# Kernel optimization log

Measured on AMD Instinct MI355X. Metric: run time of the kernel, lower is better.

Reference implementation:

```python
import jax, jax.numpy as jnp
import numpy as np

D = 1024        # d_hidden
DE = 512        # d_expert (routed)
E = 8           # n_routed_experts
TOP_K = 2
DS = DE * 2     # shared expert width = d_expert * n_shared_experts


def setup_inputs() -> dict:
    key = jax.random.key(0)
    ks = jax.random.split(key, 8)
    s = 1.0 / np.sqrt(D)
    return {
        "x": jax.random.normal(ks[0], (2, 1024, D), dtype=jnp.float32),
        "W_g": jax.random.normal(ks[1], (D, E), dtype=jnp.float32) * s,
        "Wg_e": jax.random.normal(ks[2], (E, D, DE), dtype=jnp.float32) * s,
        "Wu_e": jax.random.normal(ks[3], (E, D, DE), dtype=jnp.float32) * s,
        "Wd_e": jax.random.normal(ks[4], (E, DE, D), dtype=jnp.float32) * (1.0 / np.sqrt(DE)),
        "Wg_s": jax.random.normal(ks[5], (D, DS), dtype=jnp.float32) * s,
        "Wu_s": jax.random.normal(ks[6], (D, DS), dtype=jnp.float32) * s,
        "Wd_s": jax.random.normal(ks[7], (DS, D), dtype=jnp.float32) * (1.0 / np.sqrt(DS)),
    }


def _moe(x, W_g, Wg_e, Wu_e, Wd_e, Wg_s, Wu_s, Wd_s):
    B, T, Dm = x.shape
    N = B * T
    xf = x.reshape(N, Dm)

    # shared expert (SwiGLU)
    shared = (jax.nn.silu(xf @ Wg_s) * (xf @ Wu_s)) @ Wd_s  # [N, D]

    # gating: softmax then top-k (set membership identical to torch sorted=False)
    probs = jax.nn.softmax(xf @ W_g, axis=-1)               # [N, E]
    topk_vals, topk_ids = jax.lax.top_k(probs, TOP_K)       # [N, K]

    # combine weights c[n, e] = sum of topk_vals where routed to expert e
    # (equivalent to the original gather -> weighted scatter_add combine)
    c = jnp.zeros((N, E), dtype=x.dtype)
    c = c.at[jnp.arange(N)[:, None], topk_ids].add(topk_vals)

    # dense per-expert SwiGLU, weighted-combined (same math as gather/scatter loop)
    gate = jax.nn.silu(jnp.einsum('nd,edh->neh', xf, Wg_e))
    up = jnp.einsum('nd,edh->neh', xf, Wu_e)
    routed = jnp.einsum('neh,ne,ehd->nd', gate * up, c, Wd_e)  # [N, D]

    return (shared + routed).reshape(B, T, Dm)


def reference(x, W_g, Wg_e, Wu_e, Wd_e, Wg_s, Wu_s, Wd_s):
    return _moe(x, W_g, Wg_e, Wu_e, Wd_e, Wg_s, Wu_s, Wd_s)
```

## Files before the change

### kernel.cpp

```cpp
#include <hip/hip_runtime.h>
#include <hip/hip_bf16.h>

#define NTOK 2048
#define DIM  1024
#define DEXP 512
#define NEXP 8
#define DSH  1024
#define KH   5120
#define MAXROWS 5120
#define PACKBLOCKS 2560

typedef __hip_bfloat16 bf16;
typedef __attribute__((ext_vector_type(8))) short bf16x8;
typedef __attribute__((ext_vector_type(4))) float floatx4;

__device__ __forceinline__ void gl_lds16(const bf16* g, bf16* l) {
    __builtin_amdgcn_global_load_lds(
        (const __attribute__((address_space(1))) void*)g,
        (__attribute__((address_space(3))) void*)l, 16, 0, 0);
}

__device__ __forceinline__ float b2f(short s) {
    union { float f; unsigned u; } v;
    v.u = ((unsigned)(unsigned short)s) << 16;
    return v.f;
}

struct B4 { bf16 a, b, c, d; };

__global__ __launch_bounds__(128) void pack_gate(
        const float* __restrict__ Wg_s, const float* __restrict__ Wu_s,
        const float* __restrict__ Wg_e, const float* __restrict__ Wu_e,
        const float* __restrict__ x, const float* __restrict__ Wg,
        bf16* __restrict__ Bg, bf16* __restrict__ Bu,
        bf16* __restrict__ Xb, int2* __restrict__ te, float2* __restrict__ tp) {
    int b = blockIdx.x;
    const int tid = threadIdx.x;
    if (b < PACKBLOCKS) {
        __shared__ unsigned lt[64][35];
        const float* src; bf16* dst; int C; long dstBase; int tilesX;
        if (b < 256)        { src = Wg_s; dst = Bg; C = 1024; dstBase = 0; tilesX = 16; }
        else if (b < 1280)  { int z = (b - 256) >> 7; b = (b - 256) & 127;
                              src = Wg_e + (long)z * DIM * DEXP; dst = Bg; C = 512;
                              dstBase = (long)(DSH + z * DEXP) * 1024; tilesX = 8; }
        else if (b < 1536)  { b -= 1280; src = Wu_s; dst = Bu; C = 1024; dstBase = 0; tilesX = 16; }
        else                { int z = (b - 1536) >> 7; b = (b - 1536) & 127;
                              src = Wu_e + (long)z * DIM * DEXP; dst = Bu; C = 512;
                              dstBase = (long)(DSH + z * DEXP) * 1024; tilesX = 8; }
        const int tileX = b & (tilesX - 1), tileY = b / tilesX;
        const int c0 = tileX * 64, r0 = tileY * 64;

        const int lrow = tid >> 4, lch = tid & 15;
#pragma unroll
        for (int i = 0; i < 8; i++) {
            int row = lrow + i * 8;
            float4 v = *(const float4*)(src + (long)(r0 + row) * C + c0 + lch * 4);
            union { bf16 h[2]; unsigned u; } p0, p1;
            p0.h[0] = __float2bfloat16(v.x); p0.h[1] = __float2bfloat16(v.y);
            p1.h[0] = __float2bfloat16(v.z); p1.h[1] = __float2bfloat16(v.w);
            lt[row][lch * 2]     = p0.u;
            lt[row][lch * 2 + 1] = p1.u;
        }
        __syncthreads();
        const int kc = tid & 7;
#pragma unroll
        for (int i = 0; i < 4; i++) {
            int h = (tid >> 3) + i * 16;
            union { unsigned short s[8]; bf16x8 v8; } o;
#pragma unroll
            for (int j = 0; j < 8; j++)
                o.s[j] = ((const unsigned short*)lt[kc * 8 + j])[h];
            *(bf16x8*)(dst + dstBase + (long)(c0 + h) * 1024 + r0 + kc * 8) = o.v8;
        }
    } else {
        int t = (b - PACKBLOCKS) * 2 + (tid >> 6);
        int lane = tid & 63;
        const float* xr = x + (long)t * DIM;
        bf16* xo = Xb + (long)t * DIM;
        float acc[NEXP] = {0.f, 0.f, 0.f, 0.f, 0.f, 0.f, 0.f, 0.f};
#pragma unroll
        for (int i = 0; i < 4; i++) {
            int d = lane * 4 + i * 256;
            float4 xv = *(const float4*)(xr + d);
            B4 o{__float2bfloat16(xv.x), __float2bfloat16(xv.y),
                 __float2bfloat16(xv.z), __float2bfloat16(xv.w)};
            *(B4*)(xo + d) = o;
#pragma unroll
            for (int j = 0; j < 4; j++) {
                float xs = (j == 0) ? xv.x : (j == 1) ? xv.y : (j == 2) ? xv.z : xv.w;
                float4 w0 = *(const float4*)(Wg + (d + j) * NEXP);
                float4 w1 = *(const float4*)(Wg + (d + j) * NEXP + 4);
                acc[0] += xs * w0.x; acc[1] += xs * w0.y; acc[2] += xs * w0.z; acc[3] += xs * w0.w;
                acc[4] += xs * w1.x; acc[5] += xs * w1.y; acc[6] += xs * w1.z; acc[7] += xs * w1.w;
            }
        }
#pragma unroll
        for (int e = 0; e < NEXP; e++)
#pragma unroll
            for (int off = 32; off; off >>= 1)
                acc[e] += __shfl_xor(acc[e], off);
        if (lane == 0) {
            float m = acc[0];
#pragma unroll
            for (int e = 1; e < NEXP; e++) m = fmaxf(m, acc[e]);
            float p[NEXP], s = 0.f;
#pragma unroll
            for (int e = 0; e < NEXP; e++) { p[e] = expf(acc[e] - m); s += p[e]; }
            float inv = 1.f / s;
#pragma unroll
            for (int e = 0; e < NEXP; e++) p[e] *= inv;
            int i1 = 0;
#pragma unroll
            for (int e = 1; e < NEXP; e++) if (p[e] > p[i1]) i1 = e;
            int i2 = (i1 == 0) ? 1 : 0;
#pragma unroll
            for (int e = 0; e < NEXP; e++) if (e != i1 && p[e] > p[i2]) i2 = e;
            te[t] = make_int2(i1, i2);
            tp[t] = make_float2(p[i1], p[i2]);
        }
    }
}

__global__ __launch_bounds__(512) void assign_kernel(const int2* __restrict__ te,
                                                     const float2* __restrict__ tp,
                                                     int* __restrict__ counts,
                                                     int* __restrict__ offs,
                                                     int* __restrict__ tok_list,
                                                     float* __restrict__ cw,
                                                     int* __restrict__ s1a,
                                                     int* __restrict__ s2a) {
    __shared__ int cnt[NEXP];
    const int e = threadIdx.x >> 6;
    const int lane = threadIdx.x & 63;
    int base = 0;
    for (int t0 = 0; t0 < NTOK; t0 += 64) {
        int t = t0 + lane;
        int2 ee = te[t];
        bool m1 = (ee.x == e), m2 = (ee.y == e);
        bool mt = m1 || m2;
        unsigned long long mask = __ballot(mt);
        int pre = __popcll(mask & ((1ull << lane) - 1ull));
        if (mt) {
            int slot = base + pre;
            tok_list[e * NTOK + slot] = t;
            float2 pp = tp[t];
            cw[e * NTOK + slot] = m1 ? pp.x : pp.y;
            if (m1) s1a[t] = slot; else s2a[t] = slot;
        }
        base += __popcll(mask);
    }
    int rounded = (base + 127) & ~127;
    for (int s = base + lane; s < rounded; s += 64) {
        tok_list[e * NTOK + s] = 0;
        cw[e * NTOK + s] = 0.f;
    }
    if (lane == 0) cnt[e] = base;
    __syncthreads();
    if (threadIdx.x == 0) {
        int o = 0;
#pragma unroll
        for (int i = 0; i < NEXP; i++) {
            counts[i] = cnt[i];
            offs[i] = o;
            o += (cnt[i] + 127) & ~127;
        }
    }
}

__global__ __launch_bounds__(256) void gu_all(const bf16* __restrict__ X,
                                              const bf16* __restrict__ Bg,
                                              const bf16* __restrict__ Bu,
                                              const int* __restrict__ counts,
                                              const int* __restrict__ offs,
                                              const int* __restrict__ tok_list,
                                              const float* __restrict__ cw,
                                              const float* __restrict__ Wd_s,
                                              const float* __restrict__ Wd_e,
                                              bf16* __restrict__ Bd,
                                              bf16* __restrict__ Hs,
                                              bf16* __restrict__ He) {
    __shared__ __align__(16) bf16 sA[3][128 * 32];
    __shared__ __align__(16) bf16 sBg[3][64 * 32];
    __shared__ __align__(16) bf16 sBu[3][64 * 32];

    const int b = blockIdx.x;

    if (b >= 1280) {
        unsigned* lt = (unsigned*)&sA[0][0];
        int pb = b - 1280;
        const float* src; long dstBase; int tileX, tileY;
        if (pb < 256) {
            src = Wd_s; dstBase = 0;
            tileX = pb & 15; tileY = pb >> 4;
        } else {
            int q = pb - 256; int z = q >> 7; q &= 127;
            src = Wd_e + (long)z * DEXP * DIM;
            dstBase = DSH + (long)z * DEXP;
            tileX = q & 15; tileY = q >> 4;
        }
        const int c0 = tileX * 64, r0 = tileY * 64;
        const int tid = threadIdx.x;
        const int lrow = tid >> 4, lch = tid & 15;
#pragma unroll
        for (int i = 0; i < 4; i++) {
            int row = lrow + i * 16;
            float4 v = *(const float4*)(src + (long)(r0 + row) * DIM + c0 + lch * 4);
            union { bf16 h[2]; unsigned u; } p0, p1;
            p0.h[0] = __float2bfloat16(v.x); p0.h[1] = __float2bfloat16(v.y);
            p1.h[0] = __float2bfloat16(v.z); p1.h[1] = __float2bfloat16(v.w);
            lt[row * 35 + lch * 2]     = p0.u;
            lt[row * 35 + lch * 2 + 1] = p1.u;
        }
        __syncthreads();
        const int kc = tid & 7;
#pragma unroll
        for (int i = 0; i < 2; i++) {
            int h = (tid >> 3) + i * 32;
            union { unsigned short s[8]; bf16x8 v8; } o;
#pragma unroll
            for (int j = 0; j < 8; j++)
                o.s[j] = ((const unsigned short*)(lt + (kc * 8 + j) * 35))[h];
            *(bf16x8*)(Bd + (long)(c0 + h) * KH + dstBase + r0 + kc * 8) = o.v8;
        }
        return;
    }

    const bool routed = b < 1024;
    int e = 0, m, c;
    if (routed) {
        e = b >> 7; m = (b >> 3) & 15; c = b & 7;
        if (m * 128 >= counts[e]) return;
    } else {
        int bs = b - 1024; m = bs >> 4; c = bs & 15;
    }
    const int so = routed ? offs[e] : 0;
    const int colB0 = routed ? (DSH + e * DEXP + c * 64) : c * 64;

    const int tid = threadIdx.x;
    const int wave = tid >> 6, lane = tid & 63;
    const int wr = wave >> 1, wc = wave & 1;
    const int q = lane >> 4, l15 = lane & 15;
    const int koff = (q ^ ((l15 >> 1) & 3)) * 8;

    const int r0 = tid >> 2, c4 = tid & 3;
    const int r1 = r0 + 64;
    const int c4s = c4 ^ ((r0 >> 1) & 3);
    long aRow0, aRow1;
    if (routed) {
        const int* tl = tok_list + e * NTOK + m * 128;
        aRow0 = (long)tl[r0] * DIM;
        aRow1 = (long)tl[r1] * DIM;
    } else {
        aRow0 = (long)(m * 128 + r0) * DIM;
        aRow1 = (long)(m * 128 + r1) * DIM;
    }
    const long bRow = (long)(colB0 + r0) * DIM;

    floatx4 accG[4][2], accU[4][2];
    const floatx4 z4 = {0.f, 0.f, 0.f, 0.f};
#pragma unroll
    for (int i = 0; i < 4; i++)
#pragma unroll
        for (int j = 0; j < 2; j++) { accG[i][j] = z4; accU[i][j] = z4; }

    auto stage = [&](int bb, int k0) {
        gl_lds16(X + aRow0 + k0 + c4s * 8, &sA[bb][wave * 512]);
        gl_lds16(X + aRow1 + k0 + c4s * 8, &sA[bb][2048 + wave * 512]);
        gl_lds16(Bg + bRow + k0 + c4s * 8, &sBg[bb][wave * 512]);
        gl_lds16(Bu + bRow + k0 + c4s * 8, &sBu[bb][wave * 512]);
    };
    auto compute = [&](int bb) {
        bf16x8 af[4], bgv[2], buv[2];
#pragma unroll
        for (int rt = 0; rt < 4; rt++)
            af[rt] = *(const bf16x8*)(&sA[bb][(wr * 64 + rt * 16 + l15) * 32 + koff]);
#pragma unroll
        for (int ct = 0; ct < 2; ct++) {
            int cb = (wc * 32 + ct * 16 + l15) * 32 + koff;
            bgv[ct] = *(const bf16x8*)(&sBg[bb][cb]);
            buv[ct] = *(const bf16x8*)(&sBu[bb][cb]);
        }
#pragma unroll
        for (int rt = 0; rt < 4; rt++)
#pragma unroll
            for (int ct = 0; ct < 2; ct++) {
                accG[rt][ct] = __builtin_amdgcn_mfma_f32_16x16x32_bf16(af[rt], bgv[ct], accG[rt][ct], 0, 0, 0);
                accU[rt][ct] = __builtin_amdgcn_mfma_f32_16x16x32_bf16(af[rt], buv[ct], accU[rt][ct], 0, 0, 0);
            }
    };

    const int NS = DIM / 32;
    stage(0, 0);
    stage(1, 32);
    int bb = 0;
    for (int ks = 0; ks < NS; ks++) {
        if (ks + 2 < NS) stage((bb + 2) % 3, (ks + 2) * 32);
        if (ks + 2 < NS)      asm volatile("s_waitcnt vmcnt(8)" ::: "memory");
        else if (ks + 1 < NS) asm volatile("s_waitcnt vmcnt(4)" ::: "memory");
        else                  asm volatile("s_waitcnt vmcnt(0)" ::: "memory");
        __builtin_amdgcn_s_barrier();
        asm volatile("" ::: "memory");
        compute(bb);
        asm volatile("" ::: "memory");
        __builtin_amdgcn_s_barrier();
        bb = (bb + 1) % 3;
    }

    float wv[4][4];
#pragma unroll
    for (int rt = 0; rt < 4; rt++)
#pragma unroll
        for (int r = 0; r < 4; r++) {
            int srow = wr * 64 + rt * 16 + q * 4 + r;
            wv[rt][r] = routed ? cw[e * NTOK + m * 128 + srow] : 1.0f;
        }
#pragma unroll
    for (int rt = 0; rt < 4; rt++)
#pragma unroll
        for (int ct = 0; ct < 2; ct++)
#pragma unroll
            for (int r = 0; r < 4; r++) {
                int srow = wr * 64 + rt * 16 + q * 4 + r;
                int colLoc = c * 64 + wc * 32 + ct * 16 + l15;
                float g = accG[rt][ct][r];
                float u = accU[rt][ct][r];
                float h = (g / (1.f + __expf(-g))) * u * wv[rt][r];
                if (routed)
                    He[(long)(so + m * 128 + srow) * DEXP + colLoc] = __float2bfloat16(h);
                else
                    Hs[(long)(m * 128 + srow) * DSH + colLoc] = __float2bfloat16(h);
            }
}

__global__ __launch_bounds__(256) void down_all(const bf16* __restrict__ Hs,
                                                const bf16* __restrict__ He,
                                                const bf16* __restrict__ Bd,
                                                const int* __restrict__ counts,
                                                const int* __restrict__ offs,
                                                bf16* __restrict__ Ys,
                                                bf16* __restrict__ Ys2,
                                                bf16* __restrict__ Ye) {
    __shared__ __align__(16) bf16 sA[3][128 * 32];
    __shared__ __align__(16) bf16 sB[3][64 * 32];

    const int b = blockIdx.x;
    const bool routed = b < 2048;
    int e = 0, m, cc, kh = 0;
    if (routed) {
        e = b >> 8; m = (b >> 4) & 15; cc = b & 15;
        if (m * 128 >= counts[e]) return;
    } else {
        int bs = b - 2048;
        kh = bs & 1;
        int r = bs >> 1;
        m = r >> 4; cc = r & 15;
    }
    const int so = routed ? offs[e] : 0;
    const bf16* A = routed ? He + (long)so * DEXP : Hs;
    bf16* Y = routed ? Ye + (long)so * DIM : (kh ? Ys2 : Ys);
    const int astr = routed ? DEXP : DSH;
    const int aOffK = routed ? 0 : kh * 512;
    const int ksteps = 16;
    const int kg0 = routed ? (DSH + e * DEXP) : kh * 512;

    const int tid = threadIdx.x;
    const int wave = tid >> 6, lane = tid & 63;
    const int wr = wave >> 1, wc = wave & 1;
    const int q = lane >> 4, l15 = lane & 15;
    const int koff = (q ^ ((l15 >> 1) & 3)) * 8;

    const int r0 = tid >> 2, c4 = tid & 3;
    const int r1 = r0 + 64;
    const int c4s = c4 ^ ((r0 >> 1) & 3);
    const long aRow0 = (long)(m * 128 + r0) * astr + aOffK;
    const long aRow1 = (long)(m * 128 + r1) * astr + aOffK;
    const long bRow = (long)(cc * 64 + r0) * KH + kg0;

    floatx4 acc[4][2];
    const floatx4 z4 = {0.f, 0.f, 0.f, 0.f};
#pragma unroll
    for (int i = 0; i < 4; i++)
#pragma unroll
        for (int j = 0; j < 2; j++) acc[i][j] = z4;

    auto stage = [&](int bb, int k0) {
        gl_lds16(A + aRow0 + k0 + c4s * 8, &sA[bb][wave * 512]);
        gl_lds16(A + aRow1 + k0 + c4s * 8, &sA[bb][2048 + wave * 512]);
        gl_lds16(Bd + bRow + k0 + c4s * 8, &sB[bb][wave * 512]);
    };
    auto compute = [&](int bb) {
        bf16x8 af[4], bb2[2];
#pragma unroll
        for (int rt = 0; rt < 4; rt++)
            af[rt] = *(const bf16x8*)(&sA[bb][(wr * 64 + rt * 16 + l15) * 32 + koff]);
#pragma unroll
        for (int ct = 0; ct < 2; ct++)
            bb2[ct] = *(const bf16x8*)(&sB[bb][(wc * 32 + ct * 16 + l15) * 32 + koff]);
#pragma unroll
        for (int rt = 0; rt < 4; rt++)
#pragma unroll
            for (int ct = 0; ct < 2; ct++)
                acc[rt][ct] = __builtin_amdgcn_mfma_f32_16x16x32_bf16(af[rt], bb2[ct], acc[rt][ct], 0, 0, 0);
    };

    stage(0, 0);
    stage(1, 32);
    int bb = 0;
    for (int ks = 0; ks < ksteps; ks++) {
        if (ks + 2 < ksteps) stage((bb + 2) % 3, (ks + 2) * 32);
        if (ks + 2 < ksteps)      asm volatile("s_waitcnt vmcnt(6)" ::: "memory");
        else if (ks + 1 < ksteps) asm volatile("s_waitcnt vmcnt(3)" ::: "memory");
        else                      asm volatile("s_waitcnt vmcnt(0)" ::: "memory");
        __builtin_amdgcn_s_barrier();
        asm volatile("" ::: "memory");
        compute(bb);
        asm volatile("" ::: "memory");
        __builtin_amdgcn_s_barrier();
        bb = (bb + 1) % 3;
    }

#pragma unroll
    for (int rt = 0; rt < 4; rt++)
#pragma unroll
        for (int ct = 0; ct < 2; ct++)
#pragma unroll
            for (int r = 0; r < 4; r++) {
                int srow = wr * 64 + rt * 16 + q * 4 + r;
                int mc = cc * 64 + wc * 32 + ct * 16 + l15;
                Y[(long)(m * 128 + srow) * DIM + mc] = __float2bfloat16(acc[rt][ct][r]);
            }
}

__global__ __launch_bounds__(256) void combine_kernel(const bf16* __restrict__ Ys,
                                                      const bf16* __restrict__ Ys2,
                                                      const bf16* __restrict__ Ye,
                                                      const int2* __restrict__ te,
                                                      const int* __restrict__ s1a,
                                                      const int* __restrict__ s2a,
                                                      const int* __restrict__ offs,
                                                      float* __restrict__ out) {
    int idx = blockIdx.x * 256 + threadIdx.x;
    int t = idx >> 7;
    int d = (idx & 127) * 8;
    int2 ee = te[t];
    long r1 = (long)(offs[ee.x] + s1a[t]);
    long r2 = (long)(offs[ee.y] + s2a[t]);
    bf16x8 a = *(const bf16x8*)(Ys + (long)t * DIM + d);
    bf16x8 a2 = *(const bf16x8*)(Ys2 + (long)t * DIM + d);
    bf16x8 p = *(const bf16x8*)(Ye + r1 * DIM + d);
    bf16x8 r = *(const bf16x8*)(Ye + r2 * DIM + d);
    float* o = out + (long)t * DIM + d;
#pragma unroll
    for (int i = 0; i < 8; i++)
        o[i] = b2f(a[i]) + b2f(a2[i]) + b2f(p[i]) + b2f(r[i]);
}

extern "C" void kernel_launch(void* const* d_in, const int* in_sizes, int n_in,
                              void* d_out, int out_size, void* d_ws, size_t ws_size,
                              hipStream_t stream) {
    const float* x    = (const float*)d_in[0];
    const float* W_g  = (const float*)d_in[1];
    const float* Wg_e = (const float*)d_in[2];
    const float* Wu_e = (const float*)d_in[3];
    const float* Wd_e = (const float*)d_in[4];
    const float* Wg_s = (const float*)d_in[5];
    const float* Wu_s = (const float*)d_in[6];
    const float* Wd_s = (const float*)d_in[7];
    float* out = (float*)d_out;

    bf16* Xb = (bf16*)d_ws;
    bf16* Bg = Xb + (size_t)NTOK * DIM;
    bf16* Bu = Bg + (size_t)KH * DIM;
    bf16* Bd = Bu + (size_t)KH * DIM;
    bf16* Hs = Bd + (size_t)DIM * KH;
    bf16* He = Hs + (size_t)NTOK * DSH;
    bf16* Ys = He + (size_t)MAXROWS * DEXP;
    bf16* Ys2 = Ys + (size_t)NTOK * DIM;
    bf16* Ye = Ys2 + (size_t)NTOK * DIM;
    int*  counts   = (int*)(Ye + (size_t)MAXROWS * DIM);
    int*  offs     = counts + NEXP;
    int*  tok_list = offs + NEXP;
    float* cw      = (float*)(tok_list + NEXP * NTOK);
    int*  s1a      = (int*)(cw + NEXP * NTOK);
    int*  s2a      = s1a + NTOK;
    int2* te       = (int2*)(s2a + NTOK);
    float2* tp     = (float2*)(te + NTOK);

    pack_gate<<<PACKBLOCKS + NTOK / 2, 128, 0, stream>>>(
        Wg_s, Wu_s, Wg_e, Wu_e, x, W_g, Bg, Bu, Xb, te, tp);
    assign_kernel<<<1, 512, 0, stream>>>(te, tp, counts, offs, tok_list, cw, s1a, s2a);
    gu_all<<<2560, 256, 0, stream>>>(Xb, Bg, Bu, counts, offs, tok_list, cw,
                                     Wd_s, Wd_e, Bd, Hs, He);
    down_all<<<2560, 256, 0, stream>>>(Hs, He, Bd, counts, offs, Ys, Ys2, Ye);
    combine_kernel<<<NTOK * DIM / 8 / 256, 256, 0, stream>>>(Ys, Ys2, Ye, te, s1a, s2a, offs, out);
}
```

Before: 199.1 us.

## Widen GEMM output tiles to 128x128 and switch to double buffering

Both the gate/up and down GEMM kernels now compute 128-column output tiles instead of 64, doubling per-wave accumulators and halving the block count. The LDS pipeline drops from triple to double buffering so the larger B tiles still fit in shared memory. The aim is more reuse of A fragments per MFMA and less redundant global traffic. The cost is higher register pressure (64 accumulators for gate+up), likely lower occupancy, a shallower prefetch, and fewer blocks to fill the CUs.

New measurement: 209.6 us. +5.3%, slower.

```diff
diff --git a/kernel.cpp b/kernel.cpp
--- a/kernel.cpp
+++ b/kernel.cpp
@@ -179,15 +179,15 @@
                                               bf16* __restrict__ Bd,
                                               bf16* __restrict__ Hs,
                                               bf16* __restrict__ He) {
-    __shared__ __align__(16) bf16 sA[3][128 * 32];
-    __shared__ __align__(16) bf16 sBg[3][64 * 32];
-    __shared__ __align__(16) bf16 sBu[3][64 * 32];
+    __shared__ __align__(16) bf16 sA[2][128 * 32];
+    __shared__ __align__(16) bf16 sBg[2][128 * 32];
+    __shared__ __align__(16) bf16 sBu[2][128 * 32];
 
     const int b = blockIdx.x;
 
-    if (b >= 1280) {
+    if (b >= 640) {
         unsigned* lt = (unsigned*)&sA[0][0];
-        int pb = b - 1280;
+        int pb = b - 640;
         const float* src; long dstBase; int tileX, tileY;
         if (pb < 256) {
             src = Wd_s; dstBase = 0;
@@ -225,16 +225,19 @@
         return;
     }
 
-    const bool routed = b < 1024;
+    const bool routed = b < 512;
     int e = 0, m, c;
     if (routed) {
-        e = b >> 7; m = (b >> 3) & 15; c = b & 7;
+        e = b >> 6;
+        int r = b & 63;
+        m = r >> 2; c = r & 3;
         if (m * 128 >= counts[e]) return;
     } else {
-        int bs = b - 1024; m = bs >> 4; c = bs & 15;
+        int bs = b - 512;
+        m = bs >> 3; c = bs & 7;
     }
     const int so = routed ? offs[e] : 0;
-    const int colB0 = routed ? (DSH + e * DEXP + c * 64) : c * 64;
+    const int colB0 = routed ? (DSH + e * DEXP + c * 128) : c * 128;
 
     const int tid = threadIdx.x;
     const int wave = tid >> 6, lane = tid & 63;
@@ -254,56 +257,58 @@
         aRow0 = (long)(m * 128 + r0) * DIM;
         aRow1 = (long)(m * 128 + r1) * DIM;
     }
-    const long bRow = (long)(colB0 + r0) * DIM;
-
-    floatx4 accG[4][2], accU[4][2];
+    const long bRow0 = (long)(colB0 + r0) * DIM;
+    const long bRow1 = (long)(colB0 + 64 + r0) * DIM;
+
+    floatx4 accG[4][4], accU[4][4];
     const floatx4 z4 = {0.f, 0.f, 0.f, 0.f};
 #pragma unroll
     for (int i = 0; i < 4; i++)
 #pragma unroll
-        for (int j = 0; j < 2; j++) { accG[i][j] = z4; accU[i][j] = z4; }
+        for (int j = 0; j < 4; j++) { accG[i][j] = z4; accU[i][j] = z4; }
 
     auto stage = [&](int bb, int k0) {
         gl_lds16(X + aRow0 + k0 + c4s * 8, &sA[bb][wave * 512]);
         gl_lds16(X + aRow1 + k0 + c4s * 8, &sA[bb][2048 + wave * 512]);
-        gl_lds16(Bg + bRow + k0 + c4s * 8, &sBg[bb][wave * 512]);
-        gl_lds16(Bu + bRow + k0 + c4s * 8, &sBu[bb][wave * 512]);
+        gl_lds16(Bg + bRow0 + k0 + c4s * 8, &sBg[bb][wave * 512]);
+        gl_lds16(Bg + bRow1 + k0 + c4s * 8, &sBg[bb][2048 + wave * 512]);
+        gl_lds16(Bu + bRow0 + k0 + c4s * 8, &sBu[bb][wave * 512]);
+        gl_lds16(Bu + bRow1 + k0 + c4s * 8, &sBu[bb][2048 + wave * 512]);
     };
     auto compute = [&](int bb) {
-        bf16x8 af[4], bgv[2], buv[2];
+        bf16x8 af[4];
 #pragma unroll
         for (int rt = 0; rt < 4; rt++)
             af[rt] = *(const bf16x8*)(&sA[bb][(wr * 64 + rt * 16 + l15) * 32 + koff]);
 #pragma unroll
-        for (int ct = 0; ct < 2; ct++) {
-            int cb = (wc * 32 + ct * 16 + l15) * 32 + koff;
-            bgv[ct] = *(const bf16x8*)(&sBg[bb][cb]);
-            buv[ct] = *(const bf16x8*)(&sBu[bb][cb]);
-        }
-#pragma unroll
-        for (int rt = 0; rt < 4; rt++)
-#pragma unroll
-            for (int ct = 0; ct < 2; ct++) {
-                accG[rt][ct] = __builtin_amdgcn_mfma_f32_16x16x32_bf16(af[rt], bgv[ct], accG[rt][ct], 0, 0, 0);
-                accU[rt][ct] = __builtin_amdgcn_mfma_f32_16x16x32_bf16(af[rt], buv[ct], accU[rt][ct], 0, 0, 0);
+        for (int ct = 0; ct < 4; ct++) {
+            int cb = (wc * 64 + ct * 16 + l15) * 32 + koff;
+            bf16x8 bgv = *(const bf16x8*)(&sBg[bb][cb]);
+            bf16x8 buv = *(const bf16x8*)(&sBu[bb][cb]);
+#pragma unroll
+            for (int rt = 0; rt < 4; rt++) {
+                accG[rt][ct] = __builtin_amdgcn_mfma_f32_16x16x32_bf16(af[rt], bgv, accG[rt][ct], 0, 0, 0);
+                accU[rt][ct] = __builtin_amdgcn_mfma_f32_16x16x32_bf16(af[rt], buv, accU[rt][ct], 0, 0, 0);
             }
+        }
     };
 
     const int NS = DIM / 32;
     stage(0, 0);
-    stage(1, 32);
-    int bb = 0;
+    int cur = 0;
     for (int ks = 0; ks < NS; ks++) {
-        if (ks + 2 < NS) stage((bb + 2) % 3, (ks + 2) * 32);
-        if (ks + 2 < NS)      asm volatile("s_waitcnt vmcnt(8)" ::: "memory");
-        else if (ks + 1 < NS) asm volatile("s_waitcnt vmcnt(4)" ::: "memory");
-        else                  asm volatile("s_waitcnt vmcnt(0)" ::: "memory");
+        if (ks + 1 < NS) {
+            stage(cur ^ 1, (ks + 1) * 32);
+            asm volatile("s_waitcnt vmcnt(6)" ::: "memory");
+        } else {
+            asm volatile("s_waitcnt vmcnt(0)" ::: "memory");
+        }
         __builtin_amdgcn_s_barrier();
         asm volatile("" ::: "memory");
-        compute(bb);
+        compute(cur);
         asm volatile("" ::: "memory");
         __builtin_amdgcn_s_barrier();
-        bb = (bb + 1) % 3;
+        cur ^= 1;
     }
 
     float wv[4][4];
@@ -317,11 +322,11 @@
 #pragma unroll
     for (int rt = 0; rt < 4; rt++)
 #pragma unroll
-        for (int ct = 0; ct < 2; ct++)
+        for (int ct = 0; ct < 4; ct++)
 #pragma unroll
             for (int r = 0; r < 4; r++) {
                 int srow = wr * 64 + rt * 16 + q * 4 + r;
-                int colLoc = c * 64 + wc * 32 + ct * 16 + l15;
+                int colLoc = c * 128 + wc * 64 + ct * 16 + l15;
                 float g = accG[rt][ct][r];
                 float u = accU[rt][ct][r];
                 float h = (g / (1.f + __expf(-g))) * u * wv[rt][r];
@@ -340,20 +345,22 @@
                                                 bf16* __restrict__ Ys,
                                                 bf16* __restrict__ Ys2,
                                                 bf16* __restrict__ Ye) {
-    __shared__ __align__(16) bf16 sA[3][128 * 32];
-    __shared__ __align__(16) bf16 sB[3][64 * 32];
+    __shared__ __align__(16) bf16 sA[2][128 * 32];
+    __shared__ __align__(16) bf16 sB[2][128 * 32];
 
     const int b = blockIdx.x;
-    const bool routed = b < 2048;
+    const bool routed = b < 1024;
     int e = 0, m, cc, kh = 0;
     if (routed) {
-        e = b >> 8; m = (b >> 4) & 15; cc = b & 15;
+        e = b >> 7;
+        int r = b & 127;
+        m = r >> 3; cc = r & 7;
         if (m * 128 >= counts[e]) return;
     } else {
-        int bs = b - 2048;
+        int bs = b - 1024;
         kh = bs & 1;
         int r = bs >> 1;
-        m = r >> 4; cc = r & 15;
+        m = r >> 3; cc = r & 7;
     }
     const int so = routed ? offs[e] : 0;
     const bf16* A = routed ? He + (long)so * DEXP : Hs;
@@ -374,59 +381,61 @@
     const int c4s = c4 ^ ((r0 >> 1) & 3);
     const long aRow0 = (long)(m * 128 + r0) * astr + aOffK;
     const long aRow1 = (long)(m * 128 + r1) * astr + aOffK;
-    const long bRow = (long)(cc * 64 + r0) * KH + kg0;
-
-    floatx4 acc[4][2];
+    const long bRow0 = (long)(cc * 128 + r0) * KH + kg0;
+    const long bRow1 = (long)(cc * 128 + 64 + r0) * KH + kg0;
+
+    floatx4 acc[4][4];
     const floatx4 z4 = {0.f, 0.f, 0.f, 0.f};
 #pragma unroll
     for (int i = 0; i < 4; i++)
 #pragma unroll
-        for (int j = 0; j < 2; j++) acc[i][j] = z4;
+        for (int j = 0; j < 4; j++) acc[i][j] = z4;
 
     auto stage = [&](int bb, int k0) {
         gl_lds16(A + aRow0 + k0 + c4s * 8, &sA[bb][wave * 512]);
         gl_lds16(A + aRow1 + k0 + c4s * 8, &sA[bb][2048 + wave * 512]);
-        gl_lds16(Bd + bRow + k0 + c4s * 8, &sB[bb][wave * 512]);
+        gl_lds16(Bd + bRow0 + k0 + c4s * 8, &sB[bb][wave * 512]);
+        gl_lds16(Bd + bRow1 + k0 + c4s * 8, &sB[bb][2048 + wave * 512]);
     };
     auto compute = [&](int bb) {
-        bf16x8 af[4], bb2[2];
+        bf16x8 af[4];
 #pragma unroll
         for (int rt = 0; rt < 4; rt++)
             af[rt] = *(const bf16x8*)(&sA[bb][(wr * 64 + rt * 16 + l15) * 32 + koff]);
 #pragma unroll
-        for (int ct = 0; ct < 2; ct++)
-            bb2[ct] = *(const bf16x8*)(&sB[bb][(wc * 32 + ct * 16 + l15) * 32 + koff]);
-#pragma unroll
-        for (int rt = 0; rt < 4; rt++)
-#pragma unroll
-            for (int ct = 0; ct < 2; ct++)
-                acc[rt][ct] = __builtin_amdgcn_mfma_f32_16x16x32_bf16(af[rt], bb2[ct], acc[rt][ct], 0, 0, 0);
+        for (int ct = 0; ct < 4; ct++) {
+            bf16x8 bv = *(const bf16x8*)(&sB[bb][(wc * 64 + ct * 16 + l15) * 32 + koff]);
+#pragma unroll
+            for (int rt = 0; rt < 4; rt++)
+                acc[rt][ct] = __builtin_amdgcn_mfma_f32_16x16x32_bf16(af[rt], bv, acc[rt][ct], 0, 0, 0);
+        }
     };
 
     stage(0, 0);
-    stage(1, 32);
-    int bb = 0;
+    int cur = 0;
     for (int ks = 0; ks < ksteps; ks++) {
-        if (ks + 2 < ksteps) stage((bb + 2) % 3, (ks + 2) * 32);
-        if (ks + 2 < ksteps)      asm volatile("s_waitcnt vmcnt(6)" ::: "memory");
-        else if (ks + 1 < ksteps) asm volatile("s_waitcnt vmcnt(3)" ::: "memory");
-        else                      asm volatile("s_waitcnt vmcnt(0)" ::: "memory");
+        if (ks + 1 < ksteps) {
+            stage(cur ^ 1, (ks + 1) * 32);
+            asm volatile("s_waitcnt vmcnt(4)" ::: "memory");
+        } else {
+            asm volatile("s_waitcnt vmcnt(0)" ::: "memory");
+        }
         __builtin_amdgcn_s_barrier();
         asm volatile("" ::: "memory");
-        compute(bb);
+        compute(cur);
         asm volatile("" ::: "memory");
         __builtin_amdgcn_s_barrier();
-        bb = (bb + 1) % 3;
+        cur ^= 1;
     }
 
 #pragma unroll
     for (int rt = 0; rt < 4; rt++)
 #pragma unroll
-        for (int ct = 0; ct < 2; ct++)
+        for (int ct = 0; ct < 4; ct++)
 #pragma unroll
             for (int r = 0; r < 4; r++) {
                 int srow = wr * 64 + rt * 16 + q * 4 + r;
-                int mc = cc * 64 + wc * 32 + ct * 16 + l15;
+                int mc = cc * 128 + wc * 64 + ct * 16 + l15;
                 Y[(long)(m * 128 + srow) * DIM + mc] = __float2bfloat16(acc[rt][ct][r]);
             }
 }
@@ -489,8 +498,8 @@
     pack_gate<<<PACKBLOCKS + NTOK / 2, 128, 0, stream>>>(
         Wg_s, Wu_s, Wg_e, Wu_e, x, W_g, Bg, Bu, Xb, te, tp);
     assign_kernel<<<1, 512, 0, stream>>>(te, tp, counts, offs, tok_list, cw, s1a, s2a);
-    gu_all<<<2560, 256, 0, stream>>>(Xb, Bg, Bu, counts, offs, tok_list, cw,
-                                     Wd_s, Wd_e, Bd, Hs, He);
-    down_all<<<2560, 256, 0, stream>>>(Hs, He, Bd, counts, offs, Ys, Ys2, Ye);
+    gu_all<<<640 + 1280, 256, 0, stream>>>(Xb, Bg, Bu, counts, offs, tok_list, cw,
+                                           Wd_s, Wd_e, Bd, Hs, He);
+    down_all<<<1280, 256, 0, stream>>>(Hs, He, Bd, counts, offs, Ys, Ys2, Ye);
     combine_kernel<<<NTOK * DIM / 8 / 256, 256, 0, stream>>>(Ys, Ys2, Ye, te, s1a, s2a, offs, out);
 }
```
